# Kernel optimization log

Hardware: AMD Instinct MI355X
Metric: run time of the kernel (lower is better)

Reference implementation:

```python
import jax, jax.numpy as jnp
import numpy as np

# ---- Butterworth lowpass design, identical math to scipy.signal.butter(4, 0.5, 'low') ----
ORDER = 4
WN = 4000.0 / (0.5 * 16000.0)  # = 0.5 (normalized cutoff, Nyquist = 1)
_fs2 = 4.0                      # 2 * fs with fs = 2 (scipy bilinear convention)
_warped = _fs2 * np.tan(np.pi * WN / 4.0)
# analog Butterworth prototype poles, scaled to warped cutoff
_k = np.arange(1, ORDER + 1)
_p = _warped * np.exp(1j * np.pi * (2 * _k + ORDER - 1) / (2 * ORDER))
_gain = _warped ** ORDER
# bilinear transform: poles -> digital, zeros all at z = -1
_pd = (_fs2 + _p) / (_fs2 - _p)
_kd = _gain / np.real(np.prod(_fs2 - _p))
B_COEF = np.real(_kd * np.poly(-np.ones(ORDER))).astype(np.float32)  # [b0..b4]
A_COEF = np.real(np.poly(_pd)).astype(np.float32)                   # [1, a1..a4]


def _lfilter(x):
    """Direct-form II transposed IIR, matching scipy.signal.lfilter(b, a, x).
    x: [B, T] -> y: [B, T]. State z: [B, order]."""
    b = jnp.asarray(B_COEF)
    a = jnp.asarray(A_COEF)
    bsz = x.shape[0]
    z0 = jnp.zeros((bsz, ORDER), x.dtype)

    def step(z, xt):  # z: [B, 4], xt: [B]
        y = b[0] * xt + z[:, 0]
        z_shift = jnp.concatenate([z[:, 1:], jnp.zeros((bsz, 1), z.dtype)], axis=1)
        z_new = z_shift + b[1:] * xt[:, None] - a[1:] * y[:, None]
        return z_new, y

    _, ys = jax.lax.scan(step, z0, x.T)  # scan over time: ys [T, B]
    return ys.T


def setup_inputs() -> dict:
    key = jax.random.key(0)
    x = jax.random.normal(key, (256, 65536, 1), dtype=jnp.float32)
    return {"x": x}


def reference(x):
    # Training-time layer filters with prob%; the reference implements the
    # deterministic filter branch (the expensive path being kernelized).
    y = _lfilter(x[:, :, 0])
    return y[:, :, None]
```

## Files before the change

### kernel.cpp

```cpp
#include <hip/hip_runtime.h>
#include <cmath>
#include <complex>

#ifndef M_PI
#define M_PI 3.14159265358979323846
#endif

namespace {

constexpr int NT     = 128;
constexpr int CHUNK  = 64;
constexpr int WARM   = 64;
constexpr int REGION = NT * CHUNK;
constexpr int T_LEN  = 65536;

struct Coefs { float b0, b1, b2, b3, b4, a1, a2, a3, a4; };

__device__ __forceinline__ int lds_addr4(int o, int tg) {
    return (o << 6) + ((tg ^ (o & 15)) << 2);
}

__global__ __launch_bounds__(NT, 2) void butter_kernel(
        const float* __restrict__ x, float* __restrict__ y, Coefs c) {
    __shared__ float lds[(NT + 1) * 64];

    const int tid = threadIdx.x;
    const int bpr = T_LEN / REGION;
    const int row = blockIdx.x / bpr;
    const int bir = blockIdx.x % bpr;
    const size_t base = (size_t)row * T_LEN + (size_t)bir * REGION;
    const float4* __restrict__ xin = (const float4*)(x + base);

    if (tid < WARM / 4) {
        float4 v = make_float4(0.f, 0.f, 0.f, 0.f);
        if (bir != 0) v = ((const float4*)(x + base - WARM))[tid];
        *(float4*)&lds[lds_addr4(0, tid)] = v;
    }
#pragma unroll
    for (int k = 0; k < REGION / 4 / NT; ++k) {
        int i4 = k * NT + tid;
        float4 v = xin[i4];
        int o  = (i4 >> 4) + 1;
        int tg = i4 & 15;
        *(float4*)&lds[lds_addr4(o, tg)] = v;
    }
    __syncthreads();

    float z0 = 0.f, z1 = 0.f, z2 = 0.f, z3 = 0.f;

#define STEP_Y(xv, yv)                                   \
    do {                                                 \
        yv = fmaf(c.b0, (xv), z0);                       \
        z0 = fmaf(-c.a1, (yv), fmaf(c.b1, (xv), z1));    \
        z1 = fmaf(-c.a2, (yv), fmaf(c.b2, (xv), z2));    \
        z2 = fmaf(-c.a3, (yv), fmaf(c.b3, (xv), z3));    \
        z3 = fmaf(-c.a4, (yv), c.b4 * (xv));             \
    } while (0)

#pragma unroll
    for (int tg = 0; tg < WARM / 4; ++tg) {
        float4 xv = *(const float4*)&lds[lds_addr4(tid, tg)];
        float yd;
        STEP_Y(xv.x, yd); STEP_Y(xv.y, yd); STEP_Y(xv.z, yd); STEP_Y(xv.w, yd);
        (void)yd;
    }
    __syncthreads();

#pragma unroll
    for (int tg = 0; tg < CHUNK / 4; ++tg) {
        int a = lds_addr4(tid + 1, tg);
        float4 xv = *(const float4*)&lds[a];
        float4 yv;
        STEP_Y(xv.x, yv.x); STEP_Y(xv.y, yv.y); STEP_Y(xv.z, yv.z); STEP_Y(xv.w, yv.w);
        *(float4*)&lds[a] = yv;
    }
    __syncthreads();

    float4* __restrict__ yout = (float4*)(y + base);
#pragma unroll
    for (int k = 0; k < REGION / 4 / NT; ++k) {
        int i4 = k * NT + tid;
        int o  = (i4 >> 4) + 1;
        int tg = i4 & 15;
        yout[i4] = *(const float4*)&lds[lds_addr4(o, tg)];
    }
#undef STEP_Y
}

Coefs make_coefs() {
    const int ORDER = 4;
    const double wn  = 4000.0 / (0.5 * 16000.0);
    const double fs2 = 4.0;
    const double warped = fs2 * std::tan(M_PI * wn / 4.0);
    std::complex<double> pd[4];
    std::complex<double> prod(1.0, 0.0);
    for (int k = 1; k <= ORDER; ++k) {
        double ang = M_PI * (2.0 * k + ORDER - 1.0) / (2.0 * ORDER);
        std::complex<double> p = warped * std::exp(std::complex<double>(0.0, ang));
        prod *= (fs2 - p);
        pd[k - 1] = (fs2 + p) / (fs2 - p);
    }
    double kd = std::pow(warped, ORDER) / prod.real();
    double b[5] = { kd, 4.0 * kd, 6.0 * kd, 4.0 * kd, kd };
    std::complex<double> a[5] = { {1,0}, {0,0}, {0,0}, {0,0}, {0,0} };
    for (int k = 0; k < ORDER; ++k)
        for (int j = k + 1; j >= 1; --j) a[j] -= pd[k] * a[j - 1];
    Coefs c;
    c.b0 = (float)b[0]; c.b1 = (float)b[1]; c.b2 = (float)b[2];
    c.b3 = (float)b[3]; c.b4 = (float)b[4];
    c.a1 = (float)a[1].real(); c.a2 = (float)a[2].real();
    c.a3 = (float)a[3].real(); c.a4 = (float)a[4].real();
    return c;
}

}

extern "C" void kernel_launch(void* const* d_in, const int* in_sizes, int n_in,
                              void* d_out, int out_size, void* d_ws, size_t ws_size,
                              hipStream_t stream) {
    (void)in_sizes; (void)n_in; (void)d_ws; (void)ws_size;
    const float* x = (const float*)d_in[0];
    float* y = (float*)d_out;
    Coefs c = make_coefs();
    const int nblocks = out_size / REGION;
    butter_kernel<<<nblocks, NT, 0, stream>>>(x, y, c);
}
```

Baseline: 114.0 us.

## Drop LDS staging and give each thread a shorter chunk read directly from global

The kernel no longer stages the whole region through shared memory with barriers. Each thread now loads its own 32-sample chunk, plus 32 warm-up samples, straight from global memory into registers, filters it, and writes the result directly. This halves the serial recurrence length per thread and quadruples the thread count, aiming to hide the FMA dependency-chain latency better and to remove the shared-memory traffic and syncs. In exchange, per-instruction global accesses are strided 128 B apart across lanes rather than coalesced. The shorter warm-up window may also reduce accuracy at chunk boundaries.

```diff
diff --git a/kernel.cpp b/kernel.cpp
--- a/kernel.cpp
+++ b/kernel.cpp
@@ -8,43 +8,32 @@
 
 namespace {
 
-constexpr int NT     = 128;
-constexpr int CHUNK  = 64;
-constexpr int WARM   = 64;
-constexpr int REGION = NT * CHUNK;
-constexpr int T_LEN  = 65536;
+constexpr int NT      = 256;
+constexpr int CHUNK   = 32;
+constexpr int WARM    = 32;
+constexpr int T_LEN   = 65536;
+constexpr int CPR     = T_LEN / CHUNK;
 
 struct Coefs { float b0, b1, b2, b3, b4, a1, a2, a3, a4; };
 
-__device__ __forceinline__ int lds_addr4(int o, int tg) {
-    return (o << 6) + ((tg ^ (o & 15)) << 2);
-}
+__global__ __launch_bounds__(NT) void butter_kernel(
+        const float* __restrict__ x, float* __restrict__ y, Coefs c) {
+    const int g    = blockIdx.x * NT + threadIdx.x;
+    const int row  = g >> 11;
+    const int cpos = g & (CPR - 1);
+    const size_t base = ((size_t)row << 16) + ((size_t)cpos << 5);
 
-__global__ __launch_bounds__(NT, 2) void butter_kernel(
-        const float* __restrict__ x, float* __restrict__ y, Coefs c) {
-    __shared__ float lds[(NT + 1) * 64];
-
-    const int tid = threadIdx.x;
-    const int bpr = T_LEN / REGION;
-    const int row = blockIdx.x / bpr;
-    const int bir = blockIdx.x % bpr;
-    const size_t base = (size_t)row * T_LEN + (size_t)bir * REGION;
-    const float4* __restrict__ xin = (const float4*)(x + base);
-
-    if (tid < WARM / 4) {
-        float4 v = make_float4(0.f, 0.f, 0.f, 0.f);
-        if (bir != 0) v = ((const float4*)(x + base - WARM))[tid];
-        *(float4*)&lds[lds_addr4(0, tid)] = v;
+    float4 wv[WARM / 4];
+    float4 mv[CHUNK / 4];
+    const bool has_warm = (cpos != 0);
+    if (has_warm) {
+        const float4* __restrict__ xw = (const float4*)(x + base - WARM);
+#pragma unroll
+        for (int i = 0; i < WARM / 4; ++i) wv[i] = xw[i];
     }
+    const float4* __restrict__ xm = (const float4*)(x + base);
 #pragma unroll
-    for (int k = 0; k < REGION / 4 / NT; ++k) {
-        int i4 = k * NT + tid;
-        float4 v = xin[i4];
-        int o  = (i4 >> 4) + 1;
-        int tg = i4 & 15;
-        *(float4*)&lds[lds_addr4(o, tg)] = v;
-    }
-    __syncthreads();
+    for (int i = 0; i < CHUNK / 4; ++i) mv[i] = xm[i];
 
     float z0 = 0.f, z1 = 0.f, z2 = 0.f, z3 = 0.f;
 
@@ -57,32 +46,23 @@
         z3 = fmaf(-c.a4, (yv), c.b4 * (xv));             \
     } while (0)
 
+    if (has_warm) {
 #pragma unroll
-    for (int tg = 0; tg < WARM / 4; ++tg) {
-        float4 xv = *(const float4*)&lds[lds_addr4(tid, tg)];
-        float yd;
-        STEP_Y(xv.x, yd); STEP_Y(xv.y, yd); STEP_Y(xv.z, yd); STEP_Y(xv.w, yd);
-        (void)yd;
+        for (int i = 0; i < WARM / 4; ++i) {
+            float yd;
+            STEP_Y(wv[i].x, yd); STEP_Y(wv[i].y, yd);
+            STEP_Y(wv[i].z, yd); STEP_Y(wv[i].w, yd);
+            (void)yd;
+        }
     }
-    __syncthreads();
 
+    float4* __restrict__ yo = (float4*)(y + base);
 #pragma unroll
-    for (int tg = 0; tg < CHUNK / 4; ++tg) {
-        int a = lds_addr4(tid + 1, tg);
-        float4 xv = *(const float4*)&lds[a];
-        float4 yv;
-        STEP_Y(xv.x, yv.x); STEP_Y(xv.y, yv.y); STEP_Y(xv.z, yv.z); STEP_Y(xv.w, yv.w);
-        *(float4*)&lds[a] = yv;
-    }
-    __syncthreads();
-
-    float4* __restrict__ yout = (float4*)(y + base);
-#pragma unroll
-    for (int k = 0; k < REGION / 4 / NT; ++k) {
-        int i4 = k * NT + tid;
-        int o  = (i4 >> 4) + 1;
-        int tg = i4 & 15;
-        yout[i4] = *(const float4*)&lds[lds_addr4(o, tg)];
+    for (int i = 0; i < CHUNK / 4; ++i) {
+        float4 ov;
+        STEP_Y(mv[i].x, ov.x); STEP_Y(mv[i].y, ov.y);
+        STEP_Y(mv[i].z, ov.z); STEP_Y(mv[i].w, ov.w);
+        yo[i] = ov;
     }
 #undef STEP_Y
 }
@@ -122,6 +102,7 @@
     const float* x = (const float*)d_in[0];
     float* y = (float*)d_out;
     Coefs c = make_coefs();
-    const int nblocks = out_size / REGION;
+    const int nchunks = out_size / CHUNK;
+    const int nblocks = nchunks / NT;
     butter_kernel<<<nblocks, NT, 0, stream>>>(x, y, c);
 }
```

After: 125.8 us. 1.1x slower.

## Halve per-thread chunk, double threads, preload warm-up into registers

Applied to the files above, without the earlier changes.

Changes the block from 128 threads with 64-sample chunks to 256 threads with 32-sample chunks and 32-sample warm-up, raising the occupancy hint to 5. All global loads are issued up front into registers before the LDS stores. Each thread now copies its warm-up samples from the previous thread's chunk in LDS into registers, which removes the extra warm-up row and one serial pass. The shorter warm-up risks larger error from the IIR state approximation, and the higher register use from the staged arrays may limit occupancy.

```diff
diff --git a/kernel.cpp b/kernel.cpp
--- a/kernel.cpp
+++ b/kernel.cpp
@@ -8,21 +8,21 @@
 
 namespace {
 
-constexpr int NT     = 128;
-constexpr int CHUNK  = 64;
-constexpr int WARM   = 64;
+constexpr int NT     = 256;
+constexpr int CHUNK  = 32;
+constexpr int WARM   = 32;
 constexpr int REGION = NT * CHUNK;
 constexpr int T_LEN  = 65536;
 
 struct Coefs { float b0, b1, b2, b3, b4, a1, a2, a3, a4; };
 
 __device__ __forceinline__ int lds_addr4(int o, int tg) {
-    return (o << 6) + ((tg ^ (o & 15)) << 2);
+    return (o << 5) + ((tg ^ (o & 7)) << 2);
 }
 
-__global__ __launch_bounds__(NT, 2) void butter_kernel(
+__global__ __launch_bounds__(NT, 5) void butter_kernel(
         const float* __restrict__ x, float* __restrict__ y, Coefs c) {
-    __shared__ float lds[(NT + 1) * 64];
+    __shared__ float lds[REGION];
 
     const int tid = threadIdx.x;
     const int bpr = T_LEN / REGION;
@@ -31,18 +31,31 @@
     const size_t base = (size_t)row * T_LEN + (size_t)bir * REGION;
     const float4* __restrict__ xin = (const float4*)(x + base);
 
-    if (tid < WARM / 4) {
-        float4 v = make_float4(0.f, 0.f, 0.f, 0.f);
-        if (bir != 0) v = ((const float4*)(x + base - WARM))[tid];
-        *(float4*)&lds[lds_addr4(0, tid)] = v;
+    float4 sv[8];
+#pragma unroll
+    for (int k = 0; k < 8; ++k) sv[k] = xin[k * NT + tid];
+
+    float4 wv[WARM / 4];
+    if (tid == 0) {
+#pragma unroll
+        for (int i = 0; i < WARM / 4; ++i) wv[i] = make_float4(0.f, 0.f, 0.f, 0.f);
+        if (bir != 0) {
+            const float4* __restrict__ xw = (const float4*)(x + base - WARM);
+#pragma unroll
+            for (int i = 0; i < WARM / 4; ++i) wv[i] = xw[i];
+        }
     }
 #pragma unroll
-    for (int k = 0; k < REGION / 4 / NT; ++k) {
+    for (int k = 0; k < 8; ++k) {
         int i4 = k * NT + tid;
-        float4 v = xin[i4];
-        int o  = (i4 >> 4) + 1;
-        int tg = i4 & 15;
-        *(float4*)&lds[lds_addr4(o, tg)] = v;
+        *(float4*)&lds[lds_addr4(i4 >> 3, i4 & 7)] = sv[k];
+    }
+    __syncthreads();
+
+    if (tid != 0) {
+#pragma unroll
+        for (int tg = 0; tg < WARM / 4; ++tg)
+            wv[tg] = *(const float4*)&lds[lds_addr4(tid - 1, tg)];
     }
     __syncthreads();
 
@@ -58,33 +71,31 @@
     } while (0)
 
 #pragma unroll
-    for (int tg = 0; tg < WARM / 4; ++tg) {
-        float4 xv = *(const float4*)&lds[lds_addr4(tid, tg)];
+    for (int i = 0; i < WARM / 4; ++i) {
         float yd;
-        STEP_Y(xv.x, yd); STEP_Y(xv.y, yd); STEP_Y(xv.z, yd); STEP_Y(xv.w, yd);
+        STEP_Y(wv[i].x, yd); STEP_Y(wv[i].y, yd);
+        STEP_Y(wv[i].z, yd); STEP_Y(wv[i].w, yd);
         (void)yd;
     }
-    __syncthreads();
 
 #pragma unroll
     for (int tg = 0; tg < CHUNK / 4; ++tg) {
-        int a = lds_addr4(tid + 1, tg);
+        int a = lds_addr4(tid, tg);
         float4 xv = *(const float4*)&lds[a];
         float4 yv;
-        STEP_Y(xv.x, yv.x); STEP_Y(xv.y, yv.y); STEP_Y(xv.z, yv.z); STEP_Y(xv.w, yv.w);
+        STEP_Y(xv.x, yv.x); STEP_Y(xv.y, yv.y);
+        STEP_Y(xv.z, yv.z); STEP_Y(xv.w, yv.w);
         *(float4*)&lds[a] = yv;
     }
+#undef STEP_Y
     __syncthreads();
 
     float4* __restrict__ yout = (float4*)(y + base);
 #pragma unroll
-    for (int k = 0; k < REGION / 4 / NT; ++k) {
+    for (int k = 0; k < 8; ++k) {
         int i4 = k * NT + tid;
-        int o  = (i4 >> 4) + 1;
-        int tg = i4 & 15;
-        yout[i4] = *(const float4*)&lds[lds_addr4(o, tg)];
+        yout[i4] = *(const float4*)&lds[lds_addr4(i4 >> 3, i4 & 7)];
     }
-#undef STEP_Y
 }
 
 Coefs make_coefs() {
```

Result: faster. 111.5 us (-2.1%).
